# Performance work log

Hardware: AMD Instinct MI355X
Metric: run time of the kernel (lower is better)

Reference implementation:

```python
import jax, jax.numpy as jnp
import numpy as np

S = 2048   # sample_batch
N = 16     # num_h (agents per sample group)
OBS = 8
PRED = 12
H = 16     # hidden / embed size


def _lstm_cell(x, h, c, Wi, Wh, b):
    # torch LSTMCell gate order: i, f, g, o
    g = x @ Wi + h @ Wh + b
    i, f, gg, o = jnp.split(g, 4, axis=-1)
    c = jax.nn.sigmoid(f) * c + jax.nn.sigmoid(i) * jnp.tanh(gg)
    h = jax.nn.sigmoid(o) * jnp.tanh(c)
    return h, c


def setup_inputs() -> dict:
    key = jax.random.key(0)
    ks = jax.random.split(key, 16)
    B = S * N
    p = lambda k, sh: jax.random.normal(k, sh, jnp.float32) * 0.1
    return dict(
        traj_rel=jax.random.normal(ks[0], (OBS, B, 2), jnp.float32),
        obs_traj_pos=jax.random.normal(ks[1], (OBS, B, 2), jnp.float32),
        nei_index=jax.random.randint(ks[2], (B, N), 0, 2, jnp.int32),
        noise=jax.random.normal(ks[3], (PRED, B, 2), jnp.float32),
        enc_emb_W=p(ks[4], (2, H)), enc_emb_b=jnp.zeros((H,), jnp.float32),
        enc_Wi=p(ks[5], (H, 4 * H)), enc_Wh=p(ks[6], (H, 4 * H)), enc_b=jnp.zeros((4 * H,), jnp.float32),
        dec_in_W=p(ks[7], (H + 2, H)), dec_in_b=jnp.zeros((H,), jnp.float32),
        dec_Wi=p(ks[8], (H, 4 * H)), dec_Wh=p(ks[9], (H, 4 * H)), dec_b=jnp.zeros((4 * H,), jnp.float32),
        pool_rel_W=p(ks[10], (2, H)), pool_rel_b=jnp.zeros((H,), jnp.float32),
        pool_mlp_W=p(ks[11], (2 * H, H)), pool_mlp_b=jnp.zeros((H,), jnp.float32),
        out_W=p(ks[12], (H, 4)), out_b=jnp.zeros((4,), jnp.float32),
    )


def reference(traj_rel, obs_traj_pos, nei_index, noise,
              enc_emb_W, enc_emb_b, enc_Wi, enc_Wh, enc_b,
              dec_in_W, dec_in_b, dec_Wi, dec_Wh, dec_b,
              pool_rel_W, pool_rel_b, pool_mlp_W, pool_mlp_b,
              out_W, out_b):
    B = traj_rel.shape[1]
    mask = nei_index > 0  # (B, N)

    # --- history encoder: embed + LSTM over obs steps, take last hidden ---
    def enc_step(carry, x):
        h, c = carry
        e = jax.nn.relu(x @ enc_emb_W + enc_emb_b)
        h, c = _lstm_cell(e, h, c, enc_Wi, enc_Wh, enc_b)
        return (h, c), None

    h0 = jnp.zeros((B, H), traj_rel.dtype)
    (h_enc, _), _ = jax.lax.scan(enc_step, (h0, h0), traj_rel[:OBS])

    # --- neighbor pooling: embed relative pos, concat neighbor hidden, MLP, masked max-pool ---
    def pool(rel, h):
        re = jax.nn.relu(rel @ pool_rel_W + pool_rel_b)  # (B, N, H)
        hn = jnp.broadcast_to(h.reshape(S, 1, N, H), (S, N, N, H)).reshape(B, N, H)
        feat = jax.nn.relu(jnp.concatenate([re, hn], -1) @ pool_mlp_W + pool_mlp_b)
        masked = jnp.where(mask[..., None], feat, -1e9)
        pooled = masked.max(axis=1)  # (B, H)
        has = mask.any(axis=1, keepdims=True)
        return jnp.where(has, pooled, 0.0)

    def dec_step(carry, noise_t):
        h, c, ctx, out, pos = carry
        inp = jax.lax.stop_gradient(jnp.concatenate([ctx, out], -1))  # .detach() in torch
        e = jax.nn.relu(inp @ dec_in_W + dec_in_b)
        h, c = _lstm_cell(e, h, c, dec_Wi, dec_Wh, dec_b)
        p = pos.reshape(S, N, 2)
        # rel[s,i,j] = pos[s,i] - pos[s,j]  (matches expand/transpose subtraction)
        rel = (p[:, :, None, :] - p[:, None, :, :]).reshape(B, N, 2)
        ctx = pool(rel, h)
        o4 = (h + ctx) @ out_W + out_b
        mu = o4[:, :2]
        scale = jnp.clip(o4[:, 2:], -9.0, 4.0)
        std = jnp.exp(scale)
        pred = mu + std * noise_t
        pos = jax.lax.stop_gradient(pos + pred)
        return (h, c, ctx, pred, pos), (pred, mu, std)

    init = (h_enc, jnp.zeros_like(h_enc), jnp.zeros_like(h_enc),
            traj_rel[OBS - 1], obs_traj_pos[-1])
    _, (pred, mu, std) = jax.lax.scan(dec_step, init, noise)
    return pred, mu, std  # each (PRED, B, 2)
```

## Files before the change

kernel.cpp:

```cpp
#include <hip/hip_runtime.h>

#define S_    2048
#define N_    16
#define OBS_  8
#define PRED_ 12
#define B_    (S_*N_)
#define SCN_  2

typedef __attribute__((ext_vector_type(8))) short short8;
typedef __attribute__((ext_vector_type(4))) float floatx4;
typedef __attribute__((ext_vector_type(4))) unsigned uintx4;
typedef unsigned short ushort_t;

__device__ __forceinline__ float sigmf(float x) { return __builtin_amdgcn_rcpf(1.0f + __expf(-x)); }
__device__ __forceinline__ float tanhx(float x) { return fmaf(-2.0f, __builtin_amdgcn_rcpf(1.0f + __expf(2.0f*x)), 1.0f); }
__device__ __forceinline__ unsigned bfhi(float f) {
  return __builtin_bit_cast(unsigned, f) + 0x8000u;
}
__device__ __forceinline__ unsigned pack2bf(float lo, float hi) {
  return __builtin_amdgcn_perm(bfhi(hi), bfhi(lo), 0x07060302);
}
__device__ __forceinline__ ushort_t f2bf1(float f) { return (ushort_t)(bfhi(f) >> 16); }
__device__ __forceinline__ float rlanef(float v, int lane) {
  return __builtin_bit_cast(float, __builtin_amdgcn_readlane(__builtin_bit_cast(int, v), lane));
}

extern "C" __global__ __launch_bounds__(128, 2) void traj_ar_kernel(
    const float* __restrict__ traj_rel, const float* __restrict__ obs_pos,
    const int*  __restrict__ nei,       const float* __restrict__ noise,
    const float* __restrict__ eeW, const float* __restrict__ eeb,
    const float* __restrict__ eWi, const float* __restrict__ eWh, const float* __restrict__ eb,
    const float* __restrict__ diW, const float* __restrict__ dib,
    const float* __restrict__ dWi, const float* __restrict__ dWh, const float* __restrict__ db,
    const float* __restrict__ prW, const float* __restrict__ prb,
    const float* __restrict__ mW,  const float* __restrict__ mb,
    const float* __restrict__ oW,  const float* __restrict__ ob,
    float* __restrict__ out)
{
  __shared__ __align__(16) float h_s[SCN_][256];
  __shared__ __align__(16) float ctx_s[SCN_][256];
  __shared__ __align__(16) ushort_t e_w[SCN_][384];
  __shared__ __align__(16) ushort_t h_w[SCN_][384];
  __shared__ __align__(16) ushort_t ctx_bf[SCN_][384];
  __shared__            unsigned sm_s[SCN_][16];

  const int tid = threadIdx.x;
  const int w  = tid >> 6;
  const int l  = tid & 63;
  const int lq = l >> 4;
  const int lc = l & 15;
  const int u0 = lq*4;
  const int s  = blockIdx.x*SCN_ + w;
  const bool hi_half = (lq >= 2);

  {
    unsigned* hz = (unsigned*)h_w[w];
    unsigned* cz = (unsigned*)ctx_bf[w];
    hz[l] = 0; hz[64+l] = 0; hz[128+l] = 0;
    cz[l] = 0; cz[64+l] = 0; cz[128+l] = 0;
  }
  float POSX = obs_pos[((OBS_-1)*B_ + s*N_ + lc)*2 + 0];
  float POSY = obs_pos[((OBS_-1)*B_ + s*N_ + lc)*2 + 1];
  unsigned prevu;
  {
    float pvx = traj_rel[((OBS_-1)*B_ + s*N_ + lc)*2 + 0];
    float pvy = traj_rel[((OBS_-1)*B_ + s*N_ + lc)*2 + 1];
    prevu = pack2bf(pvx, pvy);
  }
  {
    const int a = l >> 2, nb = (l & 3)*4;
    const int4 nv = *(const int4*)&nei[(s*N_ + a)*N_ + nb];
    unsigned bits = 0;
    bits |= (nv.x > 0) ? (1u << (nb+0)) : 0u;
    bits |= (nv.y > 0) ? (1u << (nb+1)) : 0u;
    bits |= (nv.z > 0) ? (1u << (nb+2)) : 0u;
    bits |= (nv.w > 0) ? (1u << (nb+3)) : 0u;
    bits |= __shfl_xor(bits, 1, 64);
    bits |= __shfl_xor(bits, 2, 64);
    if ((l & 3) == 0) sm_s[w][a] = bits;
  }

  short8 bfrag;
  {
    uintx4 bw;
    #pragma unroll
    for (int p = 0; p < 4; ++p)
      bw[p] = pack2bf(mW[(8*lq + 2*p)*16 + lc], mW[(8*lq + 2*p + 1)*16 + lc]);
    bfrag = __builtin_bit_cast(short8, bw);
  }
  const float bm = mb[lc];

  float pWx[8], pWy[8], pB[8];
  {
    const int wu0 = (lq & 1) * 8;
    #pragma unroll
    for (int j = 0; j < 8; ++j) {
      pWx[j] = prW[wu0 + j];
      pWy[j] = prW[16 + wu0 + j];
      pB[j]  = prb[wu0 + j];
    }
  }

  float oWc[16];
  #pragma unroll
  for (int m = 0; m < 16; ++m) oWc[m] = oW[m*4 + lq];
  const float obia = ob[lq];

  float ew0[4], ew1[4], ebv[4];
  #pragma unroll
  for (int r = 0; r < 4; ++r) {
    ew0[r] = eeW[u0+r]; ew1[r] = eeW[16+u0+r]; ebv[r] = eeb[u0+r];
  }

  const int row0 = (lq & 1) * 8;

  #define LOAD_GATE_FRAG(A, C, Wi_, Wh_, bias_, g) {                                      \
    const float* gsrc_ = (lq & 2) ? (Wh_) : (Wi_);                                        \
    uintx4 aw_;                                                                           \
    aw_[0] = pack2bf(gsrc_[(row0+0)*64 + (g)*16 + lc], gsrc_[(row0+1)*64 + (g)*16 + lc]); \
    aw_[1] = pack2bf(gsrc_[(row0+2)*64 + (g)*16 + lc], gsrc_[(row0+3)*64 + (g)*16 + lc]); \
    aw_[2] = pack2bf(gsrc_[(row0+4)*64 + (g)*16 + lc], gsrc_[(row0+5)*64 + (g)*16 + lc]); \
    aw_[3] = pack2bf(gsrc_[(row0+6)*64 + (g)*16 + lc], gsrc_[(row0+7)*64 + (g)*16 + lc]); \
    (A) = __builtin_bit_cast(short8, aw_);                                                \
    (C)[0] = (bias_)[(g)*16 + u0 + 0]; (C)[1] = (bias_)[(g)*16 + u0 + 1];                 \
    (C)[2] = (bias_)[(g)*16 + u0 + 2]; (C)[3] = (bias_)[(g)*16 + u0 + 3];                 \
  }

  short8 eA0, eA1, eA2, eA3; floatx4 eC0, eC1, eC2, eC3;
  LOAD_GATE_FRAG(eA0, eC0, eWi, eWh, eb, 0);
  LOAD_GATE_FRAG(eA1, eC1, eWi, eWh, eb, 1);
  LOAD_GATE_FRAG(eA2, eC2, eWi, eWh, eb, 2);
  LOAD_GATE_FRAG(eA3, eC3, eWi, eWh, eb, 3);

  #define LSTM_EW(r, hv) {                                                            \
    float ig = sigmf(dI[r]), fg = sigmf(dF[r]), gv = tanhx(dG[r]), og = sigmf(dO[r]); \
    c4[r] = fg*c4[r] + ig*gv;                                                         \
    hv = og * tanhx(c4[r]);                                                           \
  }

  floatx4 c4 = {0.0f, 0.0f, 0.0f, 0.0f};
  const float2* xr2 = (const float2*)traj_rel;
  for (int t = 0; t < OBS_; ++t) {
    float2 x = xr2[t*B_ + s*N_ + lc];
    float e0 = fmaxf(fmaf(x.y, ew1[0], fmaf(x.x, ew0[0], ebv[0])), 0.0f);
    float e1 = fmaxf(fmaf(x.y, ew1[1], fmaf(x.x, ew0[1], ebv[1])), 0.0f);
    float e2 = fmaxf(fmaf(x.y, ew1[2], fmaf(x.x, ew0[2], ebv[2])), 0.0f);
    float e3 = fmaxf(fmaf(x.y, ew1[3], fmaf(x.x, ew0[3], ebv[3])), 0.0f);
    uint2 ep; ep.x = pack2bf(e0, e1); ep.y = pack2bf(e2, e3);
    *(uint2*)&e_w[w][lc*24 + u0] = ep;
    const ushort_t* bp = (lq < 2) ? &e_w[w][lc*24 + (lq&1)*8] : &h_w[w][lc*24 + (lq&1)*8];
    short8 bfr = *(const short8*)bp;
    floatx4 dI = __builtin_amdgcn_mfma_f32_16x16x32_bf16(eA0, bfr, eC0, 0, 0, 0);
    floatx4 dF = __builtin_amdgcn_mfma_f32_16x16x32_bf16(eA1, bfr, eC1, 0, 0, 0);
    floatx4 dG = __builtin_amdgcn_mfma_f32_16x16x32_bf16(eA2, bfr, eC2, 0, 0, 0);
    floatx4 dO = __builtin_amdgcn_mfma_f32_16x16x32_bf16(eA3, bfr, eC3, 0, 0, 0);
    float h40, h41, h42, h43;
    LSTM_EW(0, h40); LSTM_EW(1, h41); LSTM_EW(2, h42); LSTM_EW(3, h43);
    uint2 hp2; hp2.x = pack2bf(h40, h41); hp2.y = pack2bf(h42, h43);
    *(uint2*)&h_w[w][lc*24 + u0] = hp2;
  }

  short8 dA0, dA1, dA2, dA3; floatx4 dC0, dC1, dC2, dC3;
  LOAD_GATE_FRAG(dA0, dC0, dWi, dWh, db, 0);
  LOAD_GATE_FRAG(dA1, dC1, dWi, dWh, db, 1);
  LOAD_GATE_FRAG(dA2, dC2, dWi, dWh, db, 2);
  LOAD_GATE_FRAG(dA3, dC3, dWi, dWh, db, 3);

  short8 diA; floatx4 diC;
  {
    uintx4 aw; aw[0]=0; aw[1]=0; aw[2]=0; aw[3]=0;
    if (lq < 2) {
      const int r0 = lq*8;
      #pragma unroll
      for (int p = 0; p < 4; ++p)
        aw[p] = pack2bf(diW[(r0+2*p)*16 + lc], diW[(r0+2*p+1)*16 + lc]);
    } else if (lq == 2) {
      aw[0] = pack2bf(diW[16*16 + lc], diW[17*16 + lc]);
    }
    diA = __builtin_bit_cast(short8, aw);
    #pragma unroll
    for (int r = 0; r < 4; ++r) diC[r] = dib[u0 + r];
  }

  floatx4 cm[16];
  #pragma unroll
  for (int tt = 0; tt < 16; ++tt) {
    const unsigned mi = sm_s[w][tt];
    #pragma unroll
    for (int r = 0; r < 4; ++r)
      cm[tt][r] = ((mi >> (u0 + r)) & 1u) ? bm : -1e9f;
  }

  c4 = (floatx4){0.0f, 0.0f, 0.0f, 0.0f};
  const int MU_OFF = PRED_*B_*2;
  const int SD_OFF = 2*PRED_*B_*2;
  for (int t = 0; t < PRED_; ++t) {
    const float nz = noise[(t*B_ + s*N_ + lc)*2 + (lq&1)];
    float PXs[16], PYs[16];
    #pragma unroll
    for (int a2 = 0; a2 < 16; ++a2) {
      PXs[a2] = rlanef(POSX, a2);
      PYs[a2] = rlanef(POSY, a2);
    }
    {
      short8 cv = *(const short8*)&ctx_bf[w][lc*24 + (lq&1)*8];
      uintx4 pz; pz[0] = prevu; pz[1]=0; pz[2]=0; pz[3]=0;
      short8 pv = __builtin_bit_cast(short8, pz);
      short8 zz = {0,0,0,0,0,0,0,0};
      short8 bf1 = (lq < 2) ? cv : ((lq == 2) ? pv : zz);
      floatx4 d = __builtin_amdgcn_mfma_f32_16x16x32_bf16(diA, bf1, diC, 0, 0, 0);
      uint2 ep;
      ep.x = pack2bf(fmaxf(d[0],0.0f), fmaxf(d[1],0.0f));
      ep.y = pack2bf(fmaxf(d[2],0.0f), fmaxf(d[3],0.0f));
      *(uint2*)&e_w[w][lc*24 + u0] = ep;
    }
    {
      const ushort_t* bp = (lq < 2) ? &e_w[w][lc*24 + (lq&1)*8] : &h_w[w][lc*24 + (lq&1)*8];
      short8 bfr = *(const short8*)bp;
      floatx4 dI = __builtin_amdgcn_mfma_f32_16x16x32_bf16(dA0, bfr, dC0, 0, 0, 0);
      floatx4 dF = __builtin_amdgcn_mfma_f32_16x16x32_bf16(dA1, bfr, dC1, 0, 0, 0);
      floatx4 dG = __builtin_amdgcn_mfma_f32_16x16x32_bf16(dA2, bfr, dC2, 0, 0, 0);
      floatx4 dO = __builtin_amdgcn_mfma_f32_16x16x32_bf16(dA3, bfr, dC3, 0, 0, 0);
      float h40, h41, h42, h43;
      LSTM_EW(0, h40); LSTM_EW(1, h41); LSTM_EW(2, h42); LSTM_EW(3, h43);
      uint2 hp2; hp2.x = pack2bf(h40, h41); hp2.y = pack2bf(h42, h43);
      *(uint2*)&h_w[w][lc*24 + u0] = hp2;
      floatx4 hv4; hv4[0]=h40; hv4[1]=h41; hv4[2]=h42; hv4[3]=h43;
      *(floatx4*)&h_s[w][lc*16 + u0] = hv4;
    }
    const short8 hfrag = *(const short8*)&h_w[w][lc*24 + (lq&1)*8];
    {
      #pragma unroll
      for (int p = 0; p < 8; ++p) {
        const int t0 = 2*p, t1 = 2*p + 1;
        float rx0 = PXs[t0] - POSX, ry0 = PYs[t0] - POSY;
        float rx1 = PXs[t1] - POSX, ry1 = PYs[t1] - POSY;
        float rx = hi_half ? rx1 : rx0;
        float ry = hi_half ? ry1 : ry0;
        float rr[8];
        #pragma unroll
        for (int j = 0; j < 8; ++j)
          rr[j] = fmaxf(fmaf(ry, pWy[j], fmaf(rx, pWx[j], pB[j])), 0.0f);
        unsigned a0 = pack2bf(rr[0], rr[1]);
        unsigned a1 = pack2bf(rr[2], rr[3]);
        unsigned a2 = pack2bf(rr[4], rr[5]);
        unsigned a3 = pack2bf(rr[6], rr[7]);
        unsigned s0 = __shfl_xor(a0, 32, 64);
        unsigned s1 = __shfl_xor(a1, 32, 64);
        unsigned s2 = __shfl_xor(a2, 32, 64);
        unsigned s3 = __shfl_xor(a3, 32, 64);
        uintx4 f0; f0[0]=a0; f0[1]=a1; f0[2]=a2; f0[3]=a3;
        uintx4 f1; f1[0]=s0; f1[1]=s1; f1[2]=s2; f1[3]=s3;
        const short8 reA = __builtin_bit_cast(short8, f0);
        const short8 reB = __builtin_bit_cast(short8, f1);
        {
          short8 a = hi_half ? hfrag : reA;
          floatx4 d = __builtin_amdgcn_mfma_f32_16x16x32_bf16(a, bfrag, cm[t0], 0, 0, 0);
          float pm = fmaxf(fmaxf(d[0], d[1]), fmaxf(d[2], d[3]));
          pm = fmaxf(pm, __shfl_xor(pm, 16, 64));
          pm = fmaxf(pm, __shfl_xor(pm, 32, 64));
          if (lq == (t0 & 3)) {
            float cvv = fmaxf(pm, 0.0f);
            ctx_s[w][t0*16 + lc] = cvv;
            ctx_bf[w][t0*24 + lc] = f2bf1(cvv);
          }
        }
        {
          short8 a = hi_half ? hfrag : reB;
          floatx4 d = __builtin_amdgcn_mfma_f32_16x16x32_bf16(a, bfrag, cm[t1], 0, 0, 0);
          float pm = fmaxf(fmaxf(d[0], d[1]), fmaxf(d[2], d[3]));
          pm = fmaxf(pm, __shfl_xor(pm, 16, 64));
          pm = fmaxf(pm, __shfl_xor(pm, 32, 64));
          if (lq == (t1 & 3)) {
            float cvv = fmaxf(pm, 0.0f);
            ctx_s[w][t1*16 + lc] = cvv;
            ctx_bf[w][t1*24 + lc] = f2bf1(cvv);
          }
        }
      }
    }
    {
      float acc = obia;
      const floatx4* hp4 = (const floatx4*)&h_s[w][lc*16];
      const floatx4* cx4 = (const floatx4*)&ctx_s[w][lc*16];
      #pragma unroll
      for (int mm = 0; mm < 4; ++mm) {
        floatx4 hv = hp4[mm];
        floatx4 cv = cx4[mm];
        #pragma unroll
        for (int r = 0; r < 4; ++r)
          acc = fmaf(hv[r]+cv[r], oWc[mm*4+r], acc);
      }
      float sc = __shfl_down(acc, 32, 64);
      float mu = acc;
      float scale = fminf(fmaxf(sc, -9.0f), 4.0f);
      float sd = __expf(scale);
      float pr = fmaf(sd, nz, mu);
      if (lq < 2) {
        int o = (t*B_ + s*N_ + lc)*2 + lq;
        out[o]          = pr;
        out[MU_OFF + o] = mu;
        out[SD_OFF + o] = sd;
      }
      float prx = __shfl(pr, lc, 64);
      float pry = __shfl(pr, 16 + lc, 64);
      POSX += prx;
      POSY += pry;
      prevu = pack2bf(prx, pry);
    }
  }
  #undef LSTM_EW
  #undef LOAD_GATE_FRAG
}

extern "C" void kernel_launch(void* const* d_in, const int* in_sizes, int n_in,
                              void* d_out, int out_size, void* d_ws, size_t ws_size,
                              hipStream_t stream) {
  (void)in_sizes; (void)n_in; (void)d_ws; (void)ws_size; (void)out_size;
  traj_ar_kernel<<<dim3(S_/SCN_), dim3(128), 0, stream>>>(
      (const float*)d_in[0],  (const float*)d_in[1],  (const int*)d_in[2],   (const float*)d_in[3],
      (const float*)d_in[4],  (const float*)d_in[5],  (const float*)d_in[6], (const float*)d_in[7],
      (const float*)d_in[8],  (const float*)d_in[9],  (const float*)d_in[10],(const float*)d_in[11],
      (const float*)d_in[12], (const float*)d_in[13], (const float*)d_in[14],(const float*)d_in[15],
      (const float*)d_in[16], (const float*)d_in[17], (const float*)d_in[18],(const float*)d_in[19],
      (float*)d_out);
}
```

Baseline: 160.0 us.

## Pass LSTM input and hidden fragments through wave shuffles instead of LDS

Measured after the change: 160.7 us. Within noise of the previous version (+0.4%).

```diff
diff --git a/kernel.cpp b/kernel.cpp
--- a/kernel.cpp
+++ b/kernel.cpp
@@ -23,6 +23,12 @@
 __device__ __forceinline__ ushort_t f2bf1(float f) { return (ushort_t)(bfhi(f) >> 16); }
 __device__ __forceinline__ float rlanef(float v, int lane) {
   return __builtin_bit_cast(float, __builtin_amdgcn_readlane(__builtin_bit_cast(int, v), lane));
+}
+__device__ __forceinline__ unsigned shflu(unsigned v, int src) {
+  return (unsigned)__shfl((int)v, src, 64);
+}
+__device__ __forceinline__ unsigned shflxu(unsigned v, int m) {
+  return (unsigned)__shfl_xor((int)v, m, 64);
 }
 
 extern "C" __global__ __launch_bounds__(128, 2) void traj_ar_kernel(
@@ -39,8 +45,6 @@
 {
   __shared__ __align__(16) float h_s[SCN_][256];
   __shared__ __align__(16) float ctx_s[SCN_][256];
-  __shared__ __align__(16) ushort_t e_w[SCN_][384];
-  __shared__ __align__(16) ushort_t h_w[SCN_][384];
   __shared__ __align__(16) ushort_t ctx_bf[SCN_][384];
   __shared__            unsigned sm_s[SCN_][16];
 
@@ -52,11 +56,11 @@
   const int u0 = lq*4;
   const int s  = blockIdx.x*SCN_ + w;
   const bool hi_half = (lq >= 2);
-
-  {
-    unsigned* hz = (unsigned*)h_w[w];
+  const int esrc0 = (lq & 1)*32 + lc;
+  const int esrc1 = esrc0 + 16;
+
+  {
     unsigned* cz = (unsigned*)ctx_bf[w];
-    hz[l] = 0; hz[64+l] = 0; hz[128+l] = 0;
     cz[l] = 0; cz[64+l] = 0; cz[128+l] = 0;
   }
   float POSX = obs_pos[((OBS_-1)*B_ + s*N_ + lc)*2 + 0];
@@ -138,6 +142,8 @@
     hv = og * tanhx(c4[r]);                                                           \
   }
 
+  uintx4 hf; hf[0]=0; hf[1]=0; hf[2]=0; hf[3]=0;
+
   floatx4 c4 = {0.0f, 0.0f, 0.0f, 0.0f};
   const float2* xr2 = (const float2*)traj_rel;
   for (int t = 0; t < OBS_; ++t) {
@@ -147,9 +153,11 @@
     float e2 = fmaxf(fmaf(x.y, ew1[2], fmaf(x.x, ew0[2], ebv[2])), 0.0f);
     float e3 = fmaxf(fmaf(x.y, ew1[3], fmaf(x.x, ew0[3], ebv[3])), 0.0f);
     uint2 ep; ep.x = pack2bf(e0, e1); ep.y = pack2bf(e2, e3);
-    *(uint2*)&e_w[w][lc*24 + u0] = ep;
-    const ushort_t* bp = (lq < 2) ? &e_w[w][lc*24 + (lq&1)*8] : &h_w[w][lc*24 + (lq&1)*8];
-    short8 bfr = *(const short8*)bp;
+    uintx4 eu;
+    eu[0] = shflu(ep.x, esrc0); eu[1] = shflu(ep.y, esrc0);
+    eu[2] = shflu(ep.x, esrc1); eu[3] = shflu(ep.y, esrc1);
+    uintx4 bu = (lq < 2) ? eu : hf;
+    short8 bfr = __builtin_bit_cast(short8, bu);
     floatx4 dI = __builtin_amdgcn_mfma_f32_16x16x32_bf16(eA0, bfr, eC0, 0, 0, 0);
     floatx4 dF = __builtin_amdgcn_mfma_f32_16x16x32_bf16(eA1, bfr, eC1, 0, 0, 0);
     floatx4 dG = __builtin_amdgcn_mfma_f32_16x16x32_bf16(eA2, bfr, eC2, 0, 0, 0);
@@ -157,7 +165,8 @@
     float h40, h41, h42, h43;
     LSTM_EW(0, h40); LSTM_EW(1, h41); LSTM_EW(2, h42); LSTM_EW(3, h43);
     uint2 hp2; hp2.x = pack2bf(h40, h41); hp2.y = pack2bf(h42, h43);
-    *(uint2*)&h_w[w][lc*24 + u0] = hp2;
+    hf[0] = shflu(hp2.x, esrc0); hf[1] = shflu(hp2.y, esrc0);
+    hf[2] = shflu(hp2.x, esrc1); hf[3] = shflu(hp2.y, esrc1);
   }
 
   short8 dA0, dA1, dA2, dA3; floatx4 dC0, dC1, dC2, dC3;
@@ -191,6 +200,40 @@
       cm[tt][r] = ((mi >> (u0 + r)) & 1u) ? bm : -1e9f;
   }
 
+  #define MK_REFRAG(pp, F0, F1) {                                           \
+    const int t0_ = 2*(pp), t1_ = 2*(pp)+1;                                 \
+    float rx0_ = PXs[t0_] - POSX, ry0_ = PYs[t0_] - POSY;                   \
+    float rx1_ = PXs[t1_] - POSX, ry1_ = PYs[t1_] - POSY;                   \
+    float rx_ = hi_half ? rx1_ : rx0_;                                      \
+    float ry_ = hi_half ? ry1_ : ry0_;                                      \
+    float rr_[8];                                                           \
+    _Pragma("unroll")                                                       \
+    for (int j = 0; j < 8; ++j)                                             \
+      rr_[j] = fmaxf(fmaf(ry_, pWy[j], fmaf(rx_, pWx[j], pB[j])), 0.0f);    \
+    (F0)[0] = pack2bf(rr_[0], rr_[1]);                                      \
+    (F0)[1] = pack2bf(rr_[2], rr_[3]);                                      \
+    (F0)[2] = pack2bf(rr_[4], rr_[5]);                                      \
+    (F0)[3] = pack2bf(rr_[6], rr_[7]);                                      \
+    (F1)[0] = shflxu((F0)[0], 32);                                          \
+    (F1)[1] = shflxu((F0)[1], 32);                                          \
+    (F1)[2] = shflxu((F0)[2], 32);                                          \
+    (F1)[3] = shflxu((F0)[3], 32);                                          \
+  }
+
+  #define POOL_TILE(tt, FRAG) {                                             \
+    short8 a_ = hi_half ? __builtin_bit_cast(short8, hf)                    \
+                        : __builtin_bit_cast(short8, FRAG);                 \
+    floatx4 d_ = __builtin_amdgcn_mfma_f32_16x16x32_bf16(a_, bfrag, cm[tt], 0, 0, 0); \
+    float pm_ = fmaxf(fmaxf(d_[0], d_[1]), fmaxf(d_[2], d_[3]));            \
+    pm_ = fmaxf(pm_, __shfl_xor(pm_, 16, 64));                              \
+    pm_ = fmaxf(pm_, __shfl_xor(pm_, 32, 64));                              \
+    if (lq == ((tt) & 3)) {                                                 \
+      float cvv_ = fmaxf(pm_, 0.0f);                                        \
+      ctx_s[w][(tt)*16 + lc] = cvv_;                                        \
+      ctx_bf[w][(tt)*24 + lc] = f2bf1(cvv_);                                \
+    }                                                                       \
+  }
+
   c4 = (floatx4){0.0f, 0.0f, 0.0f, 0.0f};
   const int MU_OFF = PRED_*B_*2;
   const int SD_OFF = 2*PRED_*B_*2;
@@ -202,6 +245,9 @@
       PXs[a2] = rlanef(POSX, a2);
       PYs[a2] = rlanef(POSY, a2);
     }
+    uintx4 g0, g1;
+    MK_REFRAG(0, g0, g1);
+    uint2 ep;
     {
       short8 cv = *(const short8*)&ctx_bf[w][lc*24 + (lq&1)*8];
       uintx4 pz; pz[0] = prevu; pz[1]=0; pz[2]=0; pz[3]=0;
@@ -209,14 +255,15 @@
       short8 zz = {0,0,0,0,0,0,0,0};
       short8 bf1 = (lq < 2) ? cv : ((lq == 2) ? pv : zz);
       floatx4 d = __builtin_amdgcn_mfma_f32_16x16x32_bf16(diA, bf1, diC, 0, 0, 0);
-      uint2 ep;
       ep.x = pack2bf(fmaxf(d[0],0.0f), fmaxf(d[1],0.0f));
       ep.y = pack2bf(fmaxf(d[2],0.0f), fmaxf(d[3],0.0f));
-      *(uint2*)&e_w[w][lc*24 + u0] = ep;
     }
     {
-      const ushort_t* bp = (lq < 2) ? &e_w[w][lc*24 + (lq&1)*8] : &h_w[w][lc*24 + (lq&1)*8];
-      short8 bfr = *(const short8*)bp;
+      uintx4 eu;
+      eu[0] = shflu(ep.x, esrc0); eu[1] = shflu(ep.y, esrc0);
+      eu[2] = shflu(ep.x, esrc1); eu[3] = shflu(ep.y, esrc1);
+      uintx4 bu = (lq < 2) ? eu : hf;
+      short8 bfr = __builtin_bit_cast(short8, bu);
       floatx4 dI = __builtin_amdgcn_mfma_f32_16x16x32_bf16(dA0, bfr, dC0, 0, 0, 0);
       floatx4 dF = __builtin_amdgcn_mfma_f32_16x16x32_bf16(dA1, bfr, dC1, 0, 0, 0);
       floatx4 dG = __builtin_amdgcn_mfma_f32_16x16x32_bf16(dA2, bfr, dC2, 0, 0, 0);
@@ -224,59 +271,19 @@
       float h40, h41, h42, h43;
       LSTM_EW(0, h40); LSTM_EW(1, h41); LSTM_EW(2, h42); LSTM_EW(3, h43);
       uint2 hp2; hp2.x = pack2bf(h40, h41); hp2.y = pack2bf(h42, h43);
-      *(uint2*)&h_w[w][lc*24 + u0] = hp2;
+      hf[0] = shflu(hp2.x, esrc0); hf[1] = shflu(hp2.y, esrc0);
+      hf[2] = shflu(hp2.x, esrc1); hf[3] = shflu(hp2.y, esrc1);
       floatx4 hv4; hv4[0]=h40; hv4[1]=h41; hv4[2]=h42; hv4[3]=h43;
       *(floatx4*)&h_s[w][lc*16 + u0] = hv4;
     }
-    const short8 hfrag = *(const short8*)&h_w[w][lc*24 + (lq&1)*8];
     {
       #pragma unroll
       for (int p = 0; p < 8; ++p) {
-        const int t0 = 2*p, t1 = 2*p + 1;
-        float rx0 = PXs[t0] - POSX, ry0 = PYs[t0] - POSY;
-        float rx1 = PXs[t1] - POSX, ry1 = PYs[t1] - POSY;
-        float rx = hi_half ? rx1 : rx0;
-        float ry = hi_half ? ry1 : ry0;
-        float rr[8];
-        #pragma unroll
-        for (int j = 0; j < 8; ++j)
-          rr[j] = fmaxf(fmaf(ry, pWy[j], fmaf(rx, pWx[j], pB[j])), 0.0f);
-        unsigned a0 = pack2bf(rr[0], rr[1]);
-        unsigned a1 = pack2bf(rr[2], rr[3]);
-        unsigned a2 = pack2bf(rr[4], rr[5]);
-        unsigned a3 = pack2bf(rr[6], rr[7]);
-        unsigned s0 = __shfl_xor(a0, 32, 64);
-        unsigned s1 = __shfl_xor(a1, 32, 64);
-        unsigned s2 = __shfl_xor(a2, 32, 64);
-        unsigned s3 = __shfl_xor(a3, 32, 64);
-        uintx4 f0; f0[0]=a0; f0[1]=a1; f0[2]=a2; f0[3]=a3;
-        uintx4 f1; f1[0]=s0; f1[1]=s1; f1[2]=s2; f1[3]=s3;
-        const short8 reA = __builtin_bit_cast(short8, f0);
-        const short8 reB = __builtin_bit_cast(short8, f1);
-        {
-          short8 a = hi_half ? hfrag : reA;
-          floatx4 d = __builtin_amdgcn_mfma_f32_16x16x32_bf16(a, bfrag, cm[t0], 0, 0, 0);
-          float pm = fmaxf(fmaxf(d[0], d[1]), fmaxf(d[2], d[3]));
-          pm = fmaxf(pm, __shfl_xor(pm, 16, 64));
-          pm = fmaxf(pm, __shfl_xor(pm, 32, 64));
-          if (lq == (t0 & 3)) {
-            float cvv = fmaxf(pm, 0.0f);
-            ctx_s[w][t0*16 + lc] = cvv;
-            ctx_bf[w][t0*24 + lc] = f2bf1(cvv);
-          }
-        }
-        {
-          short8 a = hi_half ? hfrag : reB;
-          floatx4 d = __builtin_amdgcn_mfma_f32_16x16x32_bf16(a, bfrag, cm[t1], 0, 0, 0);
-          float pm = fmaxf(fmaxf(d[0], d[1]), fmaxf(d[2], d[3]));
-          pm = fmaxf(pm, __shfl_xor(pm, 16, 64));
-          pm = fmaxf(pm, __shfl_xor(pm, 32, 64));
-          if (lq == (t1 & 3)) {
-            float cvv = fmaxf(pm, 0.0f);
-            ctx_s[w][t1*16 + lc] = cvv;
-            ctx_bf[w][t1*24 + lc] = f2bf1(cvv);
-          }
-        }
+        uintx4 n0, n1;
+        if (p < 7) MK_REFRAG(p+1, n0, n1);
+        POOL_TILE(2*p,     g0);
+        POOL_TILE(2*p + 1, g1);
+        g0 = n0; g1 = n1;
       }
     }
     {
@@ -311,6 +318,8 @@
   }
   #undef LSTM_EW
   #undef LOAD_GATE_FRAG
+  #undef MK_REFRAG
+  #undef POOL_TILE
 }
 
 extern "C" void kernel_launch(void* const* d_in, const int* in_sizes, int n_in,
```
